# Kernel optimization log

Measured on AMD Instinct MI355X. Metric: run time of the kernel, lower is better.

Reference implementation:

```python
import jax, jax.numpy as jnp
import numpy as np

EPS = 1e-5
K = 3
N_TAP = K * K


def _bn(x, g, b, m, v):
    # eval-mode batchnorm over channel axis 1 of NCHW
    inv = g / jnp.sqrt(v + EPS)
    return x * inv[None, :, None, None] + (b - m * inv)[None, :, None, None]


def _silu(x):
    return x * jax.nn.sigmoid(x)


def _dcn(x, offset, mask, w, b, pad=1):
    """Modulated deformable conv (DCNv2), stride 1.
    x: [B,C,H,W], offset: [B,2n,H,W] ((dy,dx) per tap), mask: [B,n,H,W],
    w: [O,C,K,K], b: [O]."""
    B, C, H, W = x.shape
    O = w.shape[0]
    ky, kx = jnp.meshgrid(jnp.arange(K), jnp.arange(K), indexing='ij')
    ky = ky.reshape(N_TAP).astype(x.dtype)
    kx = kx.reshape(N_TAP).astype(x.dtype)
    off = offset.reshape(B, N_TAP, 2, H, W)
    base_y = jnp.arange(H, dtype=x.dtype)[None, None, :, None]
    base_x = jnp.arange(W, dtype=x.dtype)[None, None, None, :]
    # fractional sample positions [B,n,H,W]
    py = base_y - pad + ky[None, :, None, None] + off[:, :, 0]
    px = base_x - pad + kx[None, :, None, None] + off[:, :, 1]
    y0 = jnp.floor(py)
    x0 = jnp.floor(px)
    fy = py - y0
    fx = px - x0
    y0i = y0.astype(jnp.int32)
    x0i = x0.astype(jnp.int32)
    x_flat = x.reshape(B, C, 1, H * W)

    def corner(yi, xi, wgt):
        valid = (yi >= 0) & (yi < H) & (xi >= 0) & (xi < W)
        idx = (jnp.clip(yi, 0, H - 1) * W + jnp.clip(xi, 0, W - 1)).reshape(B, 1, N_TAP, H * W)
        v = jnp.take_along_axis(x_flat, idx, axis=-1)  # [B,C,n,HW]
        return v * (wgt * valid.astype(x.dtype)).reshape(B, 1, N_TAP, H * W)

    acc = corner(y0i, x0i, (1 - fy) * (1 - fx))
    acc = acc + corner(y0i, x0i + 1, (1 - fy) * fx)
    acc = acc + corner(y0i + 1, x0i, fy * (1 - fx))
    acc = acc + corner(y0i + 1, x0i + 1, fy * fx)
    val = acc.reshape(B, C, N_TAP, H, W) * mask[:, None]  # modulation
    out = jnp.einsum('bcnhw,ocn->bohw', val, w.reshape(O, C, N_TAP))
    return out + b[None, :, None, None]


def setup_inputs() -> dict:
    key = jax.random.key(0)
    ks = jax.random.split(key, 16)
    B, C1, H, W = 8, 256, 80, 80
    C2 = 256
    Ch = 128  # c_ = int(c2 * 0.5)
    d = {}
    d['x'] = jax.random.normal(ks[0], (B, C1, H, W), jnp.float32)
    # cv1: 1x1 conv (no bias) + BN
    d['cv1_w'] = jax.random.normal(ks[1], (Ch, C1), jnp.float32) * (1.0 / np.sqrt(C1))
    d['bn1_g'] = jax.random.uniform(ks[2], (Ch,), jnp.float32, 0.5, 1.5)
    d['bn1_b'] = jax.random.normal(ks[3], (Ch,), jnp.float32) * 0.1
    d['bn1_m'] = jax.random.normal(ks[4], (Ch,), jnp.float32) * 0.1
    d['bn1_v'] = jax.random.uniform(ks[5], (Ch,), jnp.float32, 0.5, 1.5)
    # offset/mask predictor 3x3 conv (small weights -> modest deformation)
    d['off_w'] = jax.random.normal(ks[6], (3 * N_TAP, Ch, K, K), jnp.float32) * 0.01
    d['off_b'] = jnp.zeros((3 * N_TAP,), jnp.float32)
    # dcn main weight/bias
    d['dcn_w'] = jax.random.normal(ks[7], (Ch, Ch, K, K), jnp.float32) * (1.0 / np.sqrt(Ch * N_TAP))
    d['dcn_b'] = jnp.zeros((Ch,), jnp.float32)
    d['bn2_g'] = jax.random.uniform(ks[8], (Ch,), jnp.float32, 0.5, 1.5)
    d['bn2_b'] = jax.random.normal(ks[9], (Ch,), jnp.float32) * 0.1
    d['bn2_m'] = jax.random.normal(ks[10], (Ch,), jnp.float32) * 0.1
    d['bn2_v'] = jax.random.uniform(ks[11], (Ch,), jnp.float32, 0.5, 1.5)
    # cv2: 1x1 conv (no bias) + BN
    d['cv2_w'] = jax.random.normal(ks[12], (C2, Ch), jnp.float32) * (1.0 / np.sqrt(Ch))
    d['bn3_g'] = jax.random.uniform(ks[13], (C2,), jnp.float32, 0.5, 1.5)
    d['bn3_b'] = jax.random.normal(ks[14], (C2,), jnp.float32) * 0.1
    d['bn3_m'] = jax.random.normal(ks[15], (C2,), jnp.float32) * 0.1
    d['bn3_v'] = jnp.ones((C2,), jnp.float32)
    return d


def reference(x, cv1_w, bn1_g, bn1_b, bn1_m, bn1_v,
              off_w, off_b, dcn_w, dcn_b, bn2_g, bn2_b, bn2_m, bn2_v,
              cv2_w, bn3_g, bn3_b, bn3_m, bn3_v):
    # cv1: 1x1 conv -> BN -> SiLU
    y = _silu(_bn(jnp.einsum('bchw,oc->bohw', x, cv1_w), bn1_g, bn1_b, bn1_m, bn1_v))
    # offset/mask predictor: 3x3 conv, pad 1
    raw = jax.lax.conv_general_dilated(
        y, off_w, window_strides=(1, 1), padding=((1, 1), (1, 1)),
        dimension_numbers=('NCHW', 'OIHW', 'NCHW')) + off_b[None, :, None, None]
    offset = raw[:, :2 * N_TAP]
    mask = jax.nn.sigmoid(raw[:, 2 * N_TAP:])
    # modulated deformable 3x3 conv -> BN -> SiLU
    y = _silu(_bn(_dcn(y, offset, mask, dcn_w, dcn_b), bn2_g, bn2_b, bn2_m, bn2_v))
    # cv2: 1x1 conv -> BN -> SiLU
    y = _silu(_bn(jnp.einsum('bchw,oc->bohw', y, cv2_w), bn3_g, bn3_b, bn3_m, bn3_v))
    return x + y  # shortcut (c1 == c2)
```

## Files before the change

kernel.cpp:

```cpp
#include <hip/hip_runtime.h>
#include <math.h>

#define HWSZ 6400
#define WIMG 80
#define HIMG 80
#define BEPS 1e-5f

typedef __attribute__((ext_vector_type(8))) short short8;
typedef __attribute__((ext_vector_type(4))) float f32x4;
typedef __attribute__((ext_vector_type(4))) unsigned u32x4;

__device__ __forceinline__ unsigned short f2b(float f) {
    unsigned u = __builtin_bit_cast(unsigned, f);
    u += 0x7fffu + ((u >> 16) & 1u);
    return (unsigned short)(u >> 16);
}
__device__ __forceinline__ float b2f(unsigned short h) {
    unsigned u = ((unsigned)h) << 16;
    return __builtin_bit_cast(float, u);
}
__device__ __forceinline__ float silu_f(float t) { return t / (1.f + __expf(-t)); }

__device__ __forceinline__ int remap800(int blk) { return (blk & 7) * 100 + (blk >> 3); }

__global__ __launch_bounds__(256) void k_prep(
    const float* __restrict__ cv1w, const float* __restrict__ g1, const float* __restrict__ b1,
    const float* __restrict__ m1, const float* __restrict__ v1,
    const float* __restrict__ offw, const float* __restrict__ offb,
    const float* __restrict__ dcnw, const float* __restrict__ dcnb,
    const float* __restrict__ g2, const float* __restrict__ b2,
    const float* __restrict__ m2, const float* __restrict__ v2,
    const float* __restrict__ cv2w, const float* __restrict__ g3, const float* __restrict__ b3,
    const float* __restrict__ m3, const float* __restrict__ v3,
    unsigned short* __restrict__ apk1, unsigned short* __restrict__ apko,
    unsigned short* __restrict__ apkd, unsigned short* __restrict__ apk2,
    float* __restrict__ bias1, float* __restrict__ biaso,
    float* __restrict__ bias2, float* __restrict__ bias3)
{
    int idx = blockIdx.x * 256 + threadIdx.x;
    if (idx < 32768) {
        int j = idx & 7, L = (idx >> 3) & 63, ks = (idx >> 9) & 7, mt = idx >> 12;
        int o = mt * 16 + (L & 15), k = ks * 32 + (L >> 4) * 8 + j;
        float inv = g1[o] * rsqrtf(v1[o] + BEPS);
        apk1[idx] = f2b(cv1w[o * 256 + k] * inv);
    } else if (idx < 69632) {
        int t = idx - 32768;
        int j = t & 7, L = (t >> 3) & 63;
        int mt = t / 18432, rem = t % 18432, ks = rem >> 9;
        int o = mt * 16 + (L & 15);
        int kp = ks * 32 + (L >> 4) * 8 + j;
        int n = kp >> 7, c = kp & 127;
        float wv = (o < 27) ? offw[(size_t)(o * 128 + c) * 9 + n] : 0.f;
        apko[t] = f2b(wv);
    } else if (idx < 217088) {
        int t = idx - 69632;
        int j = t & 7, L = (t >> 3) & 63;
        int mt = t / 18432, rem = t % 18432, ks = rem >> 9;
        int o = mt * 16 + (L & 15);
        int kp = ks * 32 + (L >> 4) * 8 + j;
        int n = kp >> 7, c = kp & 127;
        float inv = g2[o] * rsqrtf(v2[o] + BEPS);
        apkd[t] = f2b(dcnw[(size_t)(o * 128 + c) * 9 + n] * inv);
    } else if (idx < 249856) {
        int t = idx - 217088;
        int j = t & 7, L = (t >> 3) & 63, ks = (t >> 9) & 3, mt = t >> 11;
        int o = mt * 16 + (L & 15), k = ks * 32 + (L >> 4) * 8 + j;
        float inv = g3[o] * rsqrtf(v3[o] + BEPS);
        apk2[t] = f2b(cv2w[o * 128 + k] * inv);
    } else if (idx < 250395) {
        int t = idx - 249856;
        if (t < 128) { float inv = g1[t] * rsqrtf(v1[t] + BEPS); bias1[t] = b1[t] - m1[t] * inv; }
        else if (t < 155) { biaso[t - 128] = offb[t - 128]; }
        else if (t < 283) { int o = t - 155; float inv = g2[o] * rsqrtf(v2[o] + BEPS);
                            bias2[o] = dcnb[o] * inv + b2[o] - m2[o] * inv; }
        else { int o = t - 283; float inv = g3[o] * rsqrtf(v3[o] + BEPS); bias3[o] = b3[o] - m3[o] * inv; }
    }
}

__global__ __launch_bounds__(256) void k_cv1(
    const float* __restrict__ x, const unsigned short* __restrict__ apk1,
    const float* __restrict__ bias1, unsigned short* __restrict__ y1t)
{
    __shared__ __align__(16) unsigned short sB[20480];
    int blk = remap800(blockIdx.x);
    int b = blk / 100, pt = blk % 100;
    int p0 = pt * 64;
    int tid = threadIdx.x;
    int lane = tid & 63;
    int w = tid >> 6;
    {
        int px = lane, q = w;
        const float* xb = x + (size_t)b * 256 * HWSZ + p0 + px;
        for (int ks = 0; ks < 8; ++ks) {
            short8 v;
#pragma unroll
            for (int j = 0; j < 8; ++j)
                v[j] = (short)f2b(xb[(size_t)(ks * 32 + q * 8 + j) * HWSZ]);
            *(short8*)&sB[((ks * 4 + (px >> 4)) * 16 + (px & 15)) * 40 + q * 8] = v;
        }
    }
    __syncthreads();
    int n16 = lane & 15, qd = lane >> 4;
    f32x4 acc[2][4];
#pragma unroll
    for (int mi = 0; mi < 2; ++mi)
#pragma unroll
        for (int nt = 0; nt < 4; ++nt) acc[mi][nt] = (f32x4){0.f, 0.f, 0.f, 0.f};
    for (int ks = 0; ks < 8; ++ks) {
        short8 bf[4];
#pragma unroll
        for (int nt = 0; nt < 4; ++nt)
            bf[nt] = *(const short8*)&sB[((ks * 4 + nt) * 16 + n16) * 40 + qd * 8];
#pragma unroll
        for (int mi = 0; mi < 2; ++mi) {
            int mt = w * 2 + mi;
            short8 af = *(const short8*)&apk1[(size_t)((mt * 8 + ks) * 64 + lane) * 8];
#pragma unroll
            for (int nt = 0; nt < 4; ++nt)
                acc[mi][nt] = __builtin_amdgcn_mfma_f32_16x16x32_bf16(af, bf[nt], acc[mi][nt], 0, 0, 0);
        }
    }
    __syncthreads();
#pragma unroll
    for (int mi = 0; mi < 2; ++mi)
#pragma unroll
        for (int nt = 0; nt < 4; ++nt)
#pragma unroll
            for (int r = 0; r < 4; ++r) {
                int o = w * 32 + mi * 16 + qd * 4 + r;
                float sv = silu_f(acc[mi][nt][r] + bias1[o]);
                sB[(nt * 16 + n16) * 136 + o] = f2b(sv);
            }
    __syncthreads();
    {
        int px = tid >> 2, qq = tid & 3;
        unsigned short* ytb = y1t + ((size_t)b * HWSZ + p0 + px) * 128;
#pragma unroll
        for (int seg = 0; seg < 4; ++seg) {
            short8 v = *(const short8*)&sB[px * 136 + qq * 32 + seg * 8];
            *(short8*)&ytb[qq * 32 + seg * 8] = v;
        }
    }
}

__global__ __launch_bounds__(256) void k_off(
    const unsigned short* __restrict__ y1t, const unsigned short* __restrict__ apko,
    const float* __restrict__ biaso, float* __restrict__ raw)
{
    __shared__ __align__(16) unsigned short sV[227 * 136];
    int blk = remap800(blockIdx.x);
    int b = blk / 100, pt = blk % 100;
    int p0 = pt * 64;
    int tid = threadIdx.x;
    const unsigned short* yb = y1t + (size_t)b * HWSZ * 128;
    for (int c = tid; c < 226 * 16; c += 256) {
        int row = c >> 4, col = c & 15;
        int sp = p0 - 81 + row;
        sp = min(max(sp, 0), HWSZ - 1);
        *(short8*)&sV[row * 136 + col * 8] = *(const short8*)&yb[(size_t)sp * 128 + col * 8];
    }
    if (tid < 16) {
        short8 z = {0, 0, 0, 0, 0, 0, 0, 0};
        *(short8*)&sV[226 * 136 + tid * 8] = z;
    }
    __syncthreads();

    int lane = tid & 63, w = tid >> 6;
    int n16 = lane & 15, qd = lane >> 4;
    int p = p0 + w * 16 + n16;
    int h = p / WIMG, wx = p % WIMG;
    f32x4 acc[2];
    acc[0] = (f32x4){0.f, 0.f, 0.f, 0.f};
    acc[1] = (f32x4){0.f, 0.f, 0.f, 0.f};
#pragma unroll
    for (int n = 0; n < 9; ++n) {
        int dh = n / 3 - 1, dw = n % 3 - 1;
        int hh = h + dh, ww = wx + dw;
        bool valid = ((unsigned)hh < HIMG) && ((unsigned)ww < WIMG);
        int row = valid ? (81 + w * 16 + n16 + dh * WIMG + dw) : 226;
        const unsigned short* rV = &sV[row * 136 + qd * 8];
#pragma unroll
        for (int s = 0; s < 4; ++s) {
            int ks = n * 4 + s;
            short8 bf = *(const short8*)&rV[s * 32];
#pragma unroll
            for (int mi = 0; mi < 2; ++mi) {
                short8 af = *(const short8*)&apko[(size_t)((mi * 36 + ks) * 64 + lane) * 8];
                acc[mi] = __builtin_amdgcn_mfma_f32_16x16x32_bf16(af, bf, acc[mi], 0, 0, 0);
            }
        }
    }
    float* rb = raw + (size_t)b * 27 * HWSZ + p0 + w * 16 + n16;
#pragma unroll
    for (int mi = 0; mi < 2; ++mi)
#pragma unroll
        for (int r = 0; r < 4; ++r) {
            int o = mi * 16 + qd * 4 + r;
            if (o < 27) {
                float t = acc[mi][r] + biaso[o];
                if (o >= 18) t = 1.f / (1.f + __expf(-t));
                rb[(size_t)o * HWSZ] = t;
            }
        }
}

#define HY 12
#define HX 12
#define NHALO 144

#define ACC8(uu, cb)                                                                   \
    {                                                                                  \
        _Pragma("unroll") for (int t = 0; t < 4; ++t) {                                \
            unsigned uv = (uu)[t];                                                     \
            av[(cb) + 2 * t] = fmaf(wk, __builtin_bit_cast(float, uv << 16),           \
                                    av[(cb) + 2 * t]);                                 \
            av[(cb) + 2 * t + 1] = fmaf(wk, __builtin_bit_cast(float, uv & 0xffff0000u),\
                                        av[(cb) + 2 * t + 1]);                         \
        }                                                                              \
    }

__global__ __launch_bounds__(256, 2) void k_dcn(
    const unsigned short* __restrict__ y1t, const float* __restrict__ raw,
    const unsigned short* __restrict__ apkd, const float* __restrict__ bias2,
    unsigned short* __restrict__ zt)
{
    __shared__ __align__(16) unsigned short sH[NHALO * 128];
    __shared__ __align__(16) unsigned short sB[64 * 136];
    __shared__ float swy[2][9][64];
    __shared__ unsigned short sfx[9][64];
    __shared__ unsigned short sidx[4][9][64];

    int blk = remap800(blockIdx.x);
    int b = blk / 100, pt = blk % 100;
    int h0 = (pt / 10) * 8, w0 = (pt % 10) * 8;
    int tid = threadIdx.x;
    const unsigned short* yb = y1t + (size_t)b * HWSZ * 128;

    for (int i = tid; i < NHALO * 16; i += 256) {
        int r = i >> 4, u = i & 15;
        int ly = r / HX, lx = r % HX;
        int yy = min(max(h0 + ly - 2, 0), HIMG - 1);
        int xx = min(max(w0 + lx - 2, 0), WIMG - 1);
        *(u32x4*)&sH[r * 128 + (u ^ (r & 7)) * 8] =
            *(const u32x4*)&yb[(size_t)(yy * WIMG + xx) * 128 + u * 8];
    }
    for (int i = tid; i < 576; i += 256) {
        int n = i / 64, pp = i & 63;
        int h = h0 + (pp >> 3), wx = w0 + (pp & 7);
        int p = h * WIMG + wx;
        const float* rb = raw + (size_t)b * 27 * HWSZ + p;
        float dy = rb[(size_t)(2 * n) * HWSZ];
        float dx = rb[(size_t)(2 * n + 1) * HWSZ];
        float mk = rb[(size_t)(18 + n) * HWSZ];
        float py = (float)(h - 1 + n / 3) + dy;
        float px = (float)(wx - 1 + n % 3) + dx;
        float y0f = floorf(py), x0f = floorf(px);
        float fy = py - y0f, fx = px - x0f;
        int y0 = (int)y0f, x0 = (int)x0f;
        swy[0][n][pp] = (1.f - fy) * mk;
        swy[1][n][pp] = fy * mk;
        sfx[n][pp] = __builtin_bit_cast(unsigned short, (_Float16)fx);
#pragma unroll
        for (int k = 0; k < 4; ++k) {
            int yy = y0 + (k >> 1);
            int xx = x0 + (k & 1);
            unsigned valid = (((unsigned)yy < HIMG) && ((unsigned)xx < WIMG)) ? 0x8000u : 0u;
            int yc = min(max(yy, 0), HIMG - 1);
            int xc = min(max(xx, 0), WIMG - 1);
            sidx[k][n][pp] = (unsigned short)((yc << 7) | xc | valid);
        }
    }
    __syncthreads();

    int lane = tid & 63, w = tid >> 6;
    int n16 = lane & 15, qd = lane >> 4;
    int pxl = tid >> 2, q = tid & 3;
    f32x4 acc[2][4];
#pragma unroll
    for (int mi = 0; mi < 2; ++mi)
#pragma unroll
        for (int nt = 0; nt < 4; ++nt) acc[mi][nt] = (f32x4){0.f, 0.f, 0.f, 0.f};

    for (int n = 0; n < 9; ++n) {
        float av[32];
#pragma unroll
        for (int j = 0; j < 32; ++j) av[j] = 0.f;
        float fxv = (float)__builtin_bit_cast(_Float16, sfx[n][pxl]);
        float fx1 = 1.f - fxv;
        float wy0 = swy[0][n][pxl], wy1 = swy[1][n][pxl];
#pragma unroll
        for (int k = 0; k < 4; ++k) {
            unsigned s = sidx[k][n][pxl];
            float wk = ((k >> 1) ? wy1 : wy0) * ((k & 1) ? fxv : fx1);
            if (!(s & 0x8000u)) wk = 0.f;
            int yc = (int)((s >> 7) & 127u), xc = (int)(s & 127u);
            int ly = yc - h0 + 2, lx = xc - w0 + 2;
            if (((unsigned)ly < HY) && ((unsigned)lx < HX)) {
                int r = ly * HX + lx;
                const unsigned short* hb = &sH[r * 128];
                int xr = r & 7;
                u32x4 u0 = *(const u32x4*)&hb[((q * 4 + 0) ^ xr) * 8];
                u32x4 u1 = *(const u32x4*)&hb[((q * 4 + 1) ^ xr) * 8];
                u32x4 u2 = *(const u32x4*)&hb[((q * 4 + 2) ^ xr) * 8];
                u32x4 u3 = *(const u32x4*)&hb[((q * 4 + 3) ^ xr) * 8];
                ACC8(u0, 0) ACC8(u1, 8) ACC8(u2, 16) ACC8(u3, 24)
            } else if (wk != 0.f) {
                const unsigned short* src = &yb[(size_t)(yc * WIMG + xc) * 128 + q * 32];
                u32x4 u0 = *(const u32x4*)src;
                u32x4 u1 = *(const u32x4*)(src + 8);
                u32x4 u2 = *(const u32x4*)(src + 16);
                u32x4 u3 = *(const u32x4*)(src + 24);
                ACC8(u0, 0) ACC8(u1, 8) ACC8(u2, 16) ACC8(u3, 24)
            }
        }
        unsigned pk[16];
#pragma unroll
        for (int t = 0; t < 16; ++t)
            asm("v_cvt_pk_bf16_f32 %0, %1, %2" : "=v"(pk[t]) : "v"(av[2 * t]), "v"(av[2 * t + 1]));
        {
            unsigned short* dst = &sB[pxl * 136 + q * 32];
            *(u32x4*)dst        = (u32x4){pk[0], pk[1], pk[2], pk[3]};
            *(u32x4*)(dst + 8)  = (u32x4){pk[4], pk[5], pk[6], pk[7]};
            *(u32x4*)(dst + 16) = (u32x4){pk[8], pk[9], pk[10], pk[11]};
            *(u32x4*)(dst + 24) = (u32x4){pk[12], pk[13], pk[14], pk[15]};
        }
        __syncthreads();
#pragma unroll
        for (int sub = 0; sub < 4; ++sub) {
            int ks = n * 4 + sub;
            short8 bf[4];
#pragma unroll
            for (int nt = 0; nt < 4; ++nt)
                bf[nt] = *(const short8*)&sB[(nt * 16 + n16) * 136 + sub * 32 + qd * 8];
#pragma unroll
            for (int mi = 0; mi < 2; ++mi) {
                short8 af = *(const short8*)&apkd[(size_t)(((2 * w + mi) * 36 + ks) * 64 + lane) * 8];
#pragma unroll
                for (int nt = 0; nt < 4; ++nt)
                    acc[mi][nt] = __builtin_amdgcn_mfma_f32_16x16x32_bf16(af, bf[nt], acc[mi][nt], 0, 0, 0);
            }
        }
        __syncthreads();
    }
#pragma unroll
    for (int mi = 0; mi < 2; ++mi)
#pragma unroll
        for (int nt = 0; nt < 4; ++nt)
#pragma unroll
            for (int r = 0; r < 4; ++r) {
                int o = w * 32 + mi * 16 + qd * 4 + r;
                float sv = silu_f(acc[mi][nt][r] + bias2[o]);
                sB[(nt * 16 + n16) * 136 + o] = f2b(sv);
            }
    __syncthreads();
    {
        int px = tid >> 2, qq = tid & 3;
        int p = (h0 + (px >> 3)) * WIMG + w0 + (px & 7);
        unsigned short* zb = zt + ((size_t)b * HWSZ + p) * 128;
#pragma unroll
        for (int seg = 0; seg < 4; ++seg) {
            short8 v = *(const short8*)&sB[px * 136 + qq * 32 + seg * 8];
            *(short8*)&zb[qq * 32 + seg * 8] = v;
        }
    }
}

__global__ __launch_bounds__(256) void k_cv2(
    const unsigned short* __restrict__ zt, const float* __restrict__ x,
    const unsigned short* __restrict__ apk2, const float* __restrict__ bias3,
    float* __restrict__ out)
{
    int blk = remap800(blockIdx.x);
    int b = blk / 100, pt = blk % 100;
    int p0 = pt * 64;
    int tid = threadIdx.x;
    int lane = tid & 63, w = tid >> 6;
    int n16 = lane & 15, qd = lane >> 4;
    const unsigned short* zb = zt + ((size_t)b * HWSZ + p0) * 128;
    f32x4 acc[4][4];
#pragma unroll
    for (int mi = 0; mi < 4; ++mi)
#pragma unroll
        for (int nt = 0; nt < 4; ++nt) acc[mi][nt] = (f32x4){0.f, 0.f, 0.f, 0.f};
#pragma unroll
    for (int ks = 0; ks < 4; ++ks) {
        short8 bf[4];
#pragma unroll
        for (int nt = 0; nt < 4; ++nt)
            bf[nt] = *(const short8*)&zb[(size_t)(nt * 16 + n16) * 128 + ks * 32 + qd * 8];
#pragma unroll
        for (int mi = 0; mi < 4; ++mi) {
            int mt = w * 4 + mi;
            short8 af = *(const short8*)&apk2[(size_t)((mt * 4 + ks) * 64 + lane) * 8];
#pragma unroll
            for (int nt = 0; nt < 4; ++nt)
                acc[mi][nt] = __builtin_amdgcn_mfma_f32_16x16x32_bf16(af, bf[nt], acc[mi][nt], 0, 0, 0);
        }
    }
    const float* xb = x + (size_t)b * 256 * HWSZ;
    float* ob = out + (size_t)b * 256 * HWSZ;
#pragma unroll
    for (int mi = 0; mi < 4; ++mi)
#pragma unroll
        for (int nt = 0; nt < 4; ++nt)
#pragma unroll
            for (int r = 0; r < 4; ++r) {
                int o = w * 64 + mi * 16 + qd * 4 + r;
                size_t idx = (size_t)o * HWSZ + p0 + nt * 16 + n16;
                ob[idx] = xb[idx] + silu_f(acc[mi][nt][r] + bias3[o]);
            }
}

extern "C" void kernel_launch(void* const* d_in, const int* in_sizes, int n_in,
                              void* d_out, int out_size, void* d_ws, size_t ws_size,
                              hipStream_t stream) {
    const float* x     = (const float*)d_in[0];
    const float* cv1w  = (const float*)d_in[1];
    const float* bn1g  = (const float*)d_in[2];
    const float* bn1b  = (const float*)d_in[3];
    const float* bn1m  = (const float*)d_in[4];
    const float* bn1v  = (const float*)d_in[5];
    const float* offw  = (const float*)d_in[6];
    const float* offb  = (const float*)d_in[7];
    const float* dcnw  = (const float*)d_in[8];
    const float* dcnb  = (const float*)d_in[9];
    const float* bn2g  = (const float*)d_in[10];
    const float* bn2b  = (const float*)d_in[11];
    const float* bn2m  = (const float*)d_in[12];
    const float* bn2v  = (const float*)d_in[13];
    const float* cv2w  = (const float*)d_in[14];
    const float* bn3g  = (const float*)d_in[15];
    const float* bn3b  = (const float*)d_in[16];
    const float* bn3m  = (const float*)d_in[17];
    const float* bn3v  = (const float*)d_in[18];
    float* out = (float*)d_out;

    float* base = (float*)d_ws;
    unsigned short* y1t = (unsigned short*)base;
    float* raw   = base + 3276800;
    unsigned short* zt  = (unsigned short*)(base + 4659200);
    unsigned short* apk1 = (unsigned short*)(base + 7936000);
    unsigned short* apko = (unsigned short*)(base + 7952384);
    unsigned short* apkd = (unsigned short*)(base + 7970816);
    unsigned short* apk2 = (unsigned short*)(base + 8044544);
    float* bias1 = base + 8060928;
    float* biaso = base + 8061056;
    float* bias2 = base + 8061088;
    float* bias3 = base + 8061216;

    k_prep<<<979, 256, 0, stream>>>(cv1w, bn1g, bn1b, bn1m, bn1v,
                                    offw, offb, dcnw, dcnb,
                                    bn2g, bn2b, bn2m, bn2v,
                                    cv2w, bn3g, bn3b, bn3m, bn3v,
                                    apk1, apko, apkd, apk2,
                                    bias1, biaso, bias2, bias3);
    k_cv1<<<800, 256, 0, stream>>>(x, apk1, bias1, y1t);
    k_off<<<800, 256, 0, stream>>>(y1t, apko, biaso, raw);
    k_dcn<<<800, 256, 0, stream>>>(y1t, raw, apkd, bias2, zt);
    k_cv2<<<800, 256, 0, stream>>>(zt, x, apk2, bias3, out);
}
```

Before: 262.8 us.

## Feed DCN bilinear samples directly into MFMA registers, dropping LDS staging

In the deformable conv kernel, each lane now gathers channels in the layout the MFMA B-operand expects, so the sampled bf16 values go straight into MFMA without being written to shared memory. This removes the sB buffer and two block barriers per tap. Each wave now covers all 8 output-channel tiles for its own 16 pixels, which adds accumulator registers and more A-fragment loads from global memory. Occupancy for this kernel is raised to 3 blocks per SM. The XCD block remapping is removed from every kernel, and cv1 converts its input with packed bf16 conversion instructions.

Result: faster. 245.8 us (-6.5%).

```diff
diff --git a/kernel.cpp b/kernel.cpp
--- a/kernel.cpp
+++ b/kernel.cpp
@@ -20,8 +20,6 @@
     return __builtin_bit_cast(float, u);
 }
 __device__ __forceinline__ float silu_f(float t) { return t / (1.f + __expf(-t)); }
-
-__device__ __forceinline__ int remap800(int blk) { return (blk & 7) * 100 + (blk >> 3); }
 
 __global__ __launch_bounds__(256) void k_prep(
     const float* __restrict__ cv1w, const float* __restrict__ g1, const float* __restrict__ b1,
@@ -82,7 +80,7 @@
     const float* __restrict__ bias1, unsigned short* __restrict__ y1t)
 {
     __shared__ __align__(16) unsigned short sB[20480];
-    int blk = remap800(blockIdx.x);
+    int blk = blockIdx.x;
     int b = blk / 100, pt = blk % 100;
     int p0 = pt * 64;
     int tid = threadIdx.x;
@@ -92,11 +90,15 @@
         int px = lane, q = w;
         const float* xb = x + (size_t)b * 256 * HWSZ + p0 + px;
         for (int ks = 0; ks < 8; ++ks) {
-            short8 v;
-#pragma unroll
-            for (int j = 0; j < 8; ++j)
-                v[j] = (short)f2b(xb[(size_t)(ks * 32 + q * 8 + j) * HWSZ]);
-            *(short8*)&sB[((ks * 4 + (px >> 4)) * 16 + (px & 15)) * 40 + q * 8] = v;
+            unsigned pk[4];
+#pragma unroll
+            for (int t = 0; t < 4; ++t) {
+                float f0 = xb[(size_t)(ks * 32 + q * 8 + 2 * t) * HWSZ];
+                float f1 = xb[(size_t)(ks * 32 + q * 8 + 2 * t + 1) * HWSZ];
+                asm("v_cvt_pk_bf16_f32 %0, %1, %2" : "=v"(pk[t]) : "v"(f0), "v"(f1));
+            }
+            *(u32x4*)&sB[((ks * 4 + (px >> 4)) * 16 + (px & 15)) * 40 + q * 8] =
+                (u32x4){pk[0], pk[1], pk[2], pk[3]};
         }
     }
     __syncthreads();
@@ -148,7 +150,7 @@
     const float* __restrict__ biaso, float* __restrict__ raw)
 {
     __shared__ __align__(16) unsigned short sV[227 * 136];
-    int blk = remap800(blockIdx.x);
+    int blk = blockIdx.x;
     int b = blk / 100, pt = blk % 100;
     int p0 = pt * 64;
     int tid = threadIdx.x;
@@ -219,18 +221,17 @@
         }                                                                              \
     }
 
-__global__ __launch_bounds__(256, 2) void k_dcn(
+__global__ __launch_bounds__(256, 3) void k_dcn(
     const unsigned short* __restrict__ y1t, const float* __restrict__ raw,
     const unsigned short* __restrict__ apkd, const float* __restrict__ bias2,
     unsigned short* __restrict__ zt)
 {
     __shared__ __align__(16) unsigned short sH[NHALO * 128];
-    __shared__ __align__(16) unsigned short sB[64 * 136];
     __shared__ float swy[2][9][64];
     __shared__ unsigned short sfx[9][64];
     __shared__ unsigned short sidx[4][9][64];
 
-    int blk = remap800(blockIdx.x);
+    int blk = blockIdx.x;
     int b = blk / 100, pt = blk % 100;
     int h0 = (pt / 10) * 8, w0 = (pt % 10) * 8;
     int tid = threadIdx.x;
@@ -274,12 +275,10 @@
 
     int lane = tid & 63, w = tid >> 6;
     int n16 = lane & 15, qd = lane >> 4;
-    int pxl = tid >> 2, q = tid & 3;
-    f32x4 acc[2][4];
-#pragma unroll
-    for (int mi = 0; mi < 2; ++mi)
-#pragma unroll
-        for (int nt = 0; nt < 4; ++nt) acc[mi][nt] = (f32x4){0.f, 0.f, 0.f, 0.f};
+    int pxl = w * 16 + n16;
+    f32x4 acc[8];
+#pragma unroll
+    for (int mt = 0; mt < 8; ++mt) acc[mt] = (f32x4){0.f, 0.f, 0.f, 0.f};
 
     for (int n = 0; n < 9; ++n) {
         float av[32];
@@ -299,59 +298,47 @@
                 int r = ly * HX + lx;
                 const unsigned short* hb = &sH[r * 128];
                 int xr = r & 7;
-                u32x4 u0 = *(const u32x4*)&hb[((q * 4 + 0) ^ xr) * 8];
-                u32x4 u1 = *(const u32x4*)&hb[((q * 4 + 1) ^ xr) * 8];
-                u32x4 u2 = *(const u32x4*)&hb[((q * 4 + 2) ^ xr) * 8];
-                u32x4 u3 = *(const u32x4*)&hb[((q * 4 + 3) ^ xr) * 8];
+                u32x4 u0 = *(const u32x4*)&hb[((qd) ^ xr) * 8];
+                u32x4 u1 = *(const u32x4*)&hb[((4 + qd) ^ xr) * 8];
+                u32x4 u2 = *(const u32x4*)&hb[((8 + qd) ^ xr) * 8];
+                u32x4 u3 = *(const u32x4*)&hb[((12 + qd) ^ xr) * 8];
                 ACC8(u0, 0) ACC8(u1, 8) ACC8(u2, 16) ACC8(u3, 24)
             } else if (wk != 0.f) {
-                const unsigned short* src = &yb[(size_t)(yc * WIMG + xc) * 128 + q * 32];
+                const unsigned short* src = &yb[(size_t)(yc * WIMG + xc) * 128 + qd * 8];
                 u32x4 u0 = *(const u32x4*)src;
-                u32x4 u1 = *(const u32x4*)(src + 8);
-                u32x4 u2 = *(const u32x4*)(src + 16);
-                u32x4 u3 = *(const u32x4*)(src + 24);
+                u32x4 u1 = *(const u32x4*)(src + 32);
+                u32x4 u2 = *(const u32x4*)(src + 64);
+                u32x4 u3 = *(const u32x4*)(src + 96);
                 ACC8(u0, 0) ACC8(u1, 8) ACC8(u2, 16) ACC8(u3, 24)
             }
         }
-        unsigned pk[16];
-#pragma unroll
-        for (int t = 0; t < 16; ++t)
-            asm("v_cvt_pk_bf16_f32 %0, %1, %2" : "=v"(pk[t]) : "v"(av[2 * t]), "v"(av[2 * t + 1]));
-        {
-            unsigned short* dst = &sB[pxl * 136 + q * 32];
-            *(u32x4*)dst        = (u32x4){pk[0], pk[1], pk[2], pk[3]};
-            *(u32x4*)(dst + 8)  = (u32x4){pk[4], pk[5], pk[6], pk[7]};
-            *(u32x4*)(dst + 16) = (u32x4){pk[8], pk[9], pk[10], pk[11]};
-            *(u32x4*)(dst + 24) = (u32x4){pk[12], pk[13], pk[14], pk[15]};
-        }
-        __syncthreads();
-#pragma unroll
-        for (int sub = 0; sub < 4; ++sub) {
-            int ks = n * 4 + sub;
-            short8 bf[4];
-#pragma unroll
-            for (int nt = 0; nt < 4; ++nt)
-                bf[nt] = *(const short8*)&sB[(nt * 16 + n16) * 136 + sub * 32 + qd * 8];
-#pragma unroll
-            for (int mi = 0; mi < 2; ++mi) {
-                short8 af = *(const short8*)&apkd[(size_t)(((2 * w + mi) * 36 + ks) * 64 + lane) * 8];
-#pragma unroll
-                for (int nt = 0; nt < 4; ++nt)
-                    acc[mi][nt] = __builtin_amdgcn_mfma_f32_16x16x32_bf16(af, bf[nt], acc[mi][nt], 0, 0, 0);
-            }
-        }
-        __syncthreads();
-    }
-#pragma unroll
-    for (int mi = 0; mi < 2; ++mi)
-#pragma unroll
-        for (int nt = 0; nt < 4; ++nt)
-#pragma unroll
-            for (int r = 0; r < 4; ++r) {
-                int o = w * 32 + mi * 16 + qd * 4 + r;
-                float sv = silu_f(acc[mi][nt][r] + bias2[o]);
-                sB[(nt * 16 + n16) * 136 + o] = f2b(sv);
-            }
+#pragma unroll
+        for (int s = 0; s < 4; ++s) {
+            unsigned pk[4];
+#pragma unroll
+            for (int t = 0; t < 4; ++t)
+                asm("v_cvt_pk_bf16_f32 %0, %1, %2"
+                    : "=v"(pk[t]) : "v"(av[s * 8 + 2 * t]), "v"(av[s * 8 + 2 * t + 1]));
+            short8 bf = __builtin_bit_cast(short8, (u32x4){pk[0], pk[1], pk[2], pk[3]});
+            int ks = n * 4 + s;
+            const unsigned short* ap = apkd + (size_t)(ks * 64 + lane) * 8;
+#pragma unroll
+            for (int mt = 0; mt < 8; ++mt) {
+                short8 af = *(const short8*)&ap[(size_t)mt * 18432];
+                acc[mt] = __builtin_amdgcn_mfma_f32_16x16x32_bf16(af, bf, acc[mt], 0, 0, 0);
+            }
+        }
+    }
+    __syncthreads();
+    unsigned short* sE = sH;
+#pragma unroll
+    for (int mt = 0; mt < 8; ++mt)
+#pragma unroll
+        for (int r = 0; r < 4; ++r) {
+            int o = mt * 16 + qd * 4 + r;
+            float sv = silu_f(acc[mt][r] + bias2[o]);
+            sE[pxl * 136 + o] = f2b(sv);
+        }
     __syncthreads();
     {
         int px = tid >> 2, qq = tid & 3;
@@ -359,7 +346,7 @@
         unsigned short* zb = zt + ((size_t)b * HWSZ + p) * 128;
 #pragma unroll
         for (int seg = 0; seg < 4; ++seg) {
-            short8 v = *(const short8*)&sB[px * 136 + qq * 32 + seg * 8];
+            short8 v = *(const short8*)&sE[px * 136 + qq * 32 + seg * 8];
             *(short8*)&zb[qq * 32 + seg * 8] = v;
         }
     }
@@ -370,7 +357,7 @@
     const unsigned short* __restrict__ apk2, const float* __restrict__ bias3,
     float* __restrict__ out)
 {
-    int blk = remap800(blockIdx.x);
+    int blk = blockIdx.x;
     int b = blk / 100, pt = blk % 100;
     int p0 = pt * 64;
     int tid = threadIdx.x;
```
